# Kernel tuning notes

Hardware: AMD Instinct MI355X
Metric: run time of the kernel (lower is better)

Reference implementation:

```python
import jax, jax.numpy as jnp
import numpy as np

B, C_IN, H, W = 16, 256, 64, 64
D, K = 128, 1024  # embed_dim, nb_entries


def setup_inputs() -> dict:
    key = jax.random.key(0)
    k1, k2, k3, k4 = jax.random.split(key, 4)
    x = jax.random.normal(k1, (B, C_IN, H, W), dtype=jnp.float32)
    conv_w = jax.random.normal(k2, (C_IN, D), dtype=jnp.float32) * 0.05
    conv_b = jax.random.normal(k3, (D,), dtype=jnp.float32) * 0.05
    embed = jax.random.normal(k4, (D, K), dtype=jnp.float32)
    return {"x": x, "conv_w": conv_w, "conv_b": conv_b, "embed": embed}


def reference(x, conv_w, conv_b, embed):
    # 1x1 conv == per-pixel matmul; go straight to NHWC layout.
    z = jnp.einsum('bchw,cd->bhwd', x, conv_w) + conv_b        # [B,H,W,D]
    flat = z.reshape(-1, D)                                     # [N,D]
    # Squared-euclidean distances to codebook columns (||f||^2 - 2 f.E + ||e||^2).
    dist = (jnp.sum(flat * flat, axis=1, keepdims=True)
            - 2.0 * (flat @ embed)
            + jnp.sum(embed * embed, axis=0, keepdims=True))    # [N,K]
    embed_ind = jnp.argmin(dist, axis=1)                        # [N] int
    embed_ind = embed_ind.reshape(B, H, W)
    quantize = jnp.take(embed.T, embed_ind, axis=0)             # [B,H,W,D] gather
    diff = jnp.mean((jax.lax.stop_gradient(quantize) - z) ** 2)
    quantize = z + jax.lax.stop_gradient(quantize - z)          # straight-through
    return quantize.transpose(0, 3, 1, 2), diff, embed_ind
```

## Files before the change

### kernel.cpp

```cpp
#include <hip/hip_runtime.h>

typedef __attribute__((ext_vector_type(4))) float f32x4;
typedef __attribute__((ext_vector_type(8))) short bf16x8;

constexpr int CIN = 256;
constexpr int D   = 128;
constexpr int K   = 1024;
constexpr int HW  = 4096;
constexpr int MT  = 128;
constexpr int DIFF_OFF = 8388608;
constexpr int IDX_OFF  = 8388609;

__device__ float g_scratch[16 + K];
__device__ __align__(16) uint4 g_efrags[64 * 8 * 64];
__device__ __align__(16) uint4 g_wfrags[8 * 8 * 3 * 64];
__device__ __align__(16) float g_embedT[K * D];

__device__ inline unsigned short f2bf(float f) {
    unsigned u = __float_as_uint(f);
    u = u + 0x7fff + ((u >> 16) & 1);
    return (unsigned short)(u >> 16);
}
__device__ inline float bf2f(unsigned short h) {
    return __uint_as_float(((unsigned)h) << 16);
}
__device__ inline void split3(float v, short& a, short& b, short& c) {
    unsigned short h = f2bf(v); float r1 = v - bf2f(h);
    unsigned short m = f2bf(r1); float r2 = r1 - bf2f(m);
    a = (short)h; b = (short)m; c = (short)f2bf(r2);
}
__device__ inline void split3t(float v, short& a, short& b, short& c) {
    unsigned u1 = __float_as_uint(v) & 0xffff0000u;
    float r1 = v - __uint_as_float(u1);
    unsigned u2 = __float_as_uint(r1) & 0xffff0000u;
    float r2 = r1 - __uint_as_float(u2);
    a = (short)(u1 >> 16); b = (short)(u2 >> 16);
    c = (short)(__float_as_uint(r2) >> 16);
}

__device__ inline void gload_lds16(const uint4* g, uint4* l) {
    __builtin_amdgcn_global_load_lds(
        (const __attribute__((address_space(1))) unsigned int*)g,
        (__attribute__((address_space(3))) unsigned int*)l,
        16, 0, 0);
}

__global__ void vq_prep_all(const float* __restrict__ embed,
                            const float* __restrict__ conv_w) {
    const int bi = blockIdx.x;
    const int t  = threadIdx.x;
    if (bi < 128) {
        __shared__ float tile[32][33];
        int kb = bi >> 2, db = bi & 3;
        int tk = t & 31, td = t >> 5;
        #pragma unroll
        for (int dd = 0; dd < 4; ++dd)
            tile[td * 4 + dd][tk] =
                embed[(size_t)(db * 32 + td * 4 + dd) * K + kb * 32 + tk];
        __syncthreads();
        #pragma unroll
        for (int dd = 0; dd < 4; ++dd)
            g_embedT[(size_t)(kb * 32 + td * 4 + dd) * D + db * 32 + tk] =
                tile[tk][td * 4 + dd];
    } else if (bi < 192) {
        int kt = bi - 128, dc = t >> 6, l = t & 63;
        int k  = kt * 16 + (l & 15);
        int d0 = dc * 32 + (l >> 4) * 8;
        unsigned short hi[8], lo[8];
        #pragma unroll
        for (int j = 0; j < 8; ++j) {
            float v = embed[(size_t)(d0 + j) * K + k];
            hi[j] = f2bf(v);
            lo[j] = f2bf(v - bf2f(hi[j]));
        }
        uint4 H, L;
        H.x = (unsigned)hi[0] | ((unsigned)hi[1] << 16);
        H.y = (unsigned)hi[2] | ((unsigned)hi[3] << 16);
        H.z = (unsigned)hi[4] | ((unsigned)hi[5] << 16);
        H.w = (unsigned)hi[6] | ((unsigned)hi[7] << 16);
        L.x = (unsigned)lo[0] | ((unsigned)lo[1] << 16);
        L.y = (unsigned)lo[2] | ((unsigned)lo[3] << 16);
        L.z = (unsigned)lo[4] | ((unsigned)lo[5] << 16);
        L.w = (unsigned)lo[6] | ((unsigned)lo[7] << 16);
        g_efrags[(kt * 8 + dc * 2 + 0) * 64 + l] = H;
        g_efrags[(kt * 8 + dc * 2 + 1) * 64 + l] = L;
    } else if (bi < 208) {
        int old = (bi - 192) * 4 + (t >> 6), l = t & 63;
        int cb = old >> 3, db = old & 7;
        int c0 = cb * 32 + (l >> 4) * 8, d = db * 16 + (l & 15);
        short s1[8], s2[8], s3[8];
        #pragma unroll
        for (int j = 0; j < 8; ++j)
            split3(conv_w[(size_t)(c0 + j) * D + d], s1[j], s2[j], s3[j]);
        #pragma unroll
        for (int s = 0; s < 3; ++s) {
            const short* sp = s == 0 ? s1 : s == 1 ? s2 : s3;
            uint4 P;
            P.x = (unsigned)(unsigned short)sp[0] | ((unsigned)(unsigned short)sp[1] << 16);
            P.y = (unsigned)(unsigned short)sp[2] | ((unsigned)(unsigned short)sp[3] << 16);
            P.z = (unsigned)(unsigned short)sp[4] | ((unsigned)(unsigned short)sp[5] << 16);
            P.w = (unsigned)(unsigned short)sp[6] | ((unsigned)(unsigned short)sp[7] << 16);
            g_wfrags[((cb * 8 + db) * 3 + s) * 64 + l] = P;
        }
    } else {
        int k = (bi - 208) * 256 + t;
        if (k == 0) g_scratch[0] = 0.0f;
        float s = 0.0f;
        for (int d = 0; d < D; ++d) { float v = embed[d * K + k]; s += v * v; }
        g_scratch[16 + k] = s;
    }
}

#define MFMA(a, bb, c) __builtin_amdgcn_mfma_f32_16x16x32_bf16(a, bb, c, 0, 0, 0)

__global__ __launch_bounds__(256, 2) void vq_main(
    const float* __restrict__ x, const float* __restrict__ conv_b,
    float* __restrict__ out)
{
    __shared__ __align__(16) uint4 ebuf[4096];
    __shared__ float e2_s[K];
    __shared__ float tbuf[4 * 16 * 36];
    __shared__ int   ks_s[MT];
    __shared__ float red_s[4];

    const int t    = threadIdx.x;
    const int lane = t & 63;
    const int w    = t >> 6;
    const int wg   = blockIdx.x;
    const int n0   = wg * MT;
    const int b    = n0 >> 12;
    const int hw0  = n0 & 4095;
    const int pxb  = w * 32;
    const int lp   = lane & 15;
    const int lg   = lane >> 4;

    for (int k = t; k < K; k += 256) e2_s[k] = g_scratch[16 + k];

    f32x4 Cz[2][8];
    #pragma unroll
    for (int db = 0; db < 8; ++db) {
        float bv = conv_b[db * 16 + lp];
        Cz[0][db] = (f32x4){bv, bv, bv, bv};
        Cz[1][db] = Cz[0][db];
    }
    {
        #pragma unroll
        for (int i = 0; i < 6; ++i)
            gload_lds16(&g_wfrags[(w * 6 + i) * 64 + lane], &ebuf[(w * 6 + i) * 64]);
        asm volatile("s_waitcnt vmcnt(0)" ::: "memory");
        __syncthreads();

        const float* xl = x + (size_t)b * CIN * HW + (size_t)(lg * 8) * HW
                          + hw0 + pxb + lp;
        for (int cb = 0; cb < 8; ++cb) {
            float v[2][8];
            #pragma unroll
            for (int rb = 0; rb < 2; ++rb)
                #pragma unroll
                for (int j = 0; j < 8; ++j)
                    v[rb][j] = xl[(size_t)(cb * 32 + j) * HW + rb * 16];
            if (cb < 7) {
                const uint4* wsrc = g_wfrags + (size_t)(cb + 1) * 1536;
                uint4* wdst = ebuf + ((cb + 1) & 1) * 1536;
                #pragma unroll
                for (int i = 0; i < 6; ++i)
                    gload_lds16(&wsrc[(w * 6 + i) * 64 + lane], &wdst[(w * 6 + i) * 64]);
            }
            bf16x8 X1[2], X2[2], X3[2];
            #pragma unroll
            for (int rb = 0; rb < 2; ++rb)
                #pragma unroll
                for (int j = 0; j < 8; ++j) {
                    short a, bb, c;
                    split3t(v[rb][j], a, bb, c);
                    X1[rb][j] = a; X2[rb][j] = bb; X3[rb][j] = c;
                }
            const uint4* wb = ebuf + (cb & 1) * 1536;
            #pragma unroll
            for (int db = 0; db < 8; ++db) {
                bf16x8 W1 = *(const bf16x8*)&wb[(db * 3 + 0) * 64 + lane];
                bf16x8 W2 = *(const bf16x8*)&wb[(db * 3 + 1) * 64 + lane];
                bf16x8 W3 = *(const bf16x8*)&wb[(db * 3 + 2) * 64 + lane];
                Cz[0][db] = MFMA(X1[0], W1, Cz[0][db]);
                Cz[1][db] = MFMA(X1[1], W1, Cz[1][db]);
                Cz[0][db] = MFMA(X1[0], W2, Cz[0][db]);
                Cz[1][db] = MFMA(X1[1], W2, Cz[1][db]);
                Cz[0][db] = MFMA(X2[0], W1, Cz[0][db]);
                Cz[1][db] = MFMA(X2[1], W1, Cz[1][db]);
                Cz[0][db] = MFMA(X1[0], W3, Cz[0][db]);
                Cz[1][db] = MFMA(X1[1], W3, Cz[1][db]);
                Cz[0][db] = MFMA(X2[0], W2, Cz[0][db]);
                Cz[1][db] = MFMA(X2[1], W2, Cz[1][db]);
                Cz[0][db] = MFMA(X3[0], W1, Cz[0][db]);
                Cz[1][db] = MFMA(X3[1], W1, Cz[1][db]);
            }
            asm volatile("s_waitcnt vmcnt(0)" ::: "memory");
            __syncthreads();
        }
    }

    bf16x8 A2h[2][4], A2l[2][4];
    {
        float* tb = tbuf + w * 576;
        #pragma unroll
        for (int rb = 0; rb < 2; ++rb) {
            #pragma unroll
            for (int dc = 0; dc < 4; ++dc) {
                #pragma unroll
                for (int h = 0; h < 2; ++h)
                    #pragma unroll
                    for (int r = 0; r < 4; ++r)
                        tb[(lg * 4 + r) * 36 + h * 16 + lp] = Cz[rb][dc * 2 + h][r];
                asm volatile("s_waitcnt lgkmcnt(0)" ::: "memory");
                f32x4 a0 = *(const f32x4*)&tb[lp * 36 + lg * 8];
                f32x4 a1 = *(const f32x4*)&tb[lp * 36 + lg * 8 + 4];
                #pragma unroll
                for (int j = 0; j < 8; ++j) {
                    float zv = -2.0f * (j < 4 ? a0[j] : a1[j - 4]);
                    unsigned short hb = f2bf(zv);
                    A2h[rb][dc][j] = (short)hb;
                    A2l[rb][dc][j] = (short)f2bf(zv - bf2f(hb));
                }
                asm volatile("s_waitcnt lgkmcnt(0)" ::: "memory");
            }
        }
    }

    const uint4* gfr = g_efrags;
    {
        #pragma unroll
        for (int i = 0; i < 8; ++i)
            gload_lds16(&gfr[(w * 8 + i) * 64 + lane], &ebuf[(w * 8 + i) * 64]);
        asm volatile("s_waitcnt vmcnt(0)" ::: "memory");
        __syncthreads();
    }

    float v1[8], v2[8]; int i1[8], i2[8];
    #pragma unroll
    for (int q = 0; q < 8; ++q) { v1[q] = 3.4e38f; v2[q] = 3.4e38f; i1[q] = 0; i2[q] = 0; }

    for (int c = 0; c < 16; ++c) {
        if (c < 15) {
            const uint4* esrc = gfr + (size_t)(c + 1) * 2048;
            uint4* edst = ebuf + ((c + 1) & 1) * 2048;
            #pragma unroll
            for (int i = 0; i < 8; ++i)
                gload_lds16(&esrc[(w * 8 + i) * 64 + lane], &edst[(w * 8 + i) * 64]);
        }
        const bf16x8* eb = (const bf16x8*)&ebuf[(c & 1) * 2048];
        #pragma unroll
        for (int ktl = 0; ktl < 4; ++ktl) {
            int kt = c * 4 + ktl;
            bf16x8 Bh[4], Bl[4];
            #pragma unroll
            for (int dc = 0; dc < 4; ++dc) {
                Bh[dc] = eb[(ktl * 8 + dc * 2 + 0) * 64 + lane];
                Bl[dc] = eb[(ktl * 8 + dc * 2 + 1) * 64 + lane];
            }
            float e2v = e2_s[kt * 16 + lp];
            f32x4 C0 = (f32x4){e2v, e2v, e2v, e2v};
            f32x4 C1 = C0;
            __builtin_amdgcn_s_setprio(1);
            #pragma unroll
            for (int dc = 0; dc < 4; ++dc) {
                C0 = MFMA(A2h[0][dc], Bh[dc], C0);
                C1 = MFMA(A2h[1][dc], Bh[dc], C1);
                C0 = MFMA(A2l[0][dc], Bh[dc], C0);
                C1 = MFMA(A2l[1][dc], Bh[dc], C1);
                C0 = MFMA(A2h[0][dc], Bl[dc], C0);
                C1 = MFMA(A2h[1][dc], Bl[dc], C1);
            }
            __builtin_amdgcn_s_setprio(0);
            int kk = kt * 16 + lp;
            #pragma unroll
            for (int rb = 0; rb < 2; ++rb) {
                f32x4 C = rb ? C1 : C0;
                #pragma unroll
                for (int r = 0; r < 4; ++r) {
                    int q = rb * 4 + r;
                    float s = C[r];
                    bool lt1 = s < v1[q], lt2 = s < v2[q];
                    v2[q] = lt1 ? v1[q] : (lt2 ? s  : v2[q]);
                    i2[q] = lt1 ? i1[q] : (lt2 ? kk : i2[q]);
                    v1[q] = lt1 ? s  : v1[q];
                    i1[q] = lt1 ? kk : i1[q];
                }
            }
        }
        if (c < 15) asm volatile("s_waitcnt vmcnt(0)" ::: "memory");
        __syncthreads();
    }

    #pragma unroll
    for (int off = 1; off < 16; off <<= 1) {
        #pragma unroll
        for (int q = 0; q < 8; ++q) {
            float b1 = __shfl_xor(v1[q], off); int bi1 = __shfl_xor(i1[q], off);
            float b2 = __shfl_xor(v2[q], off); int bi2 = __shfl_xor(i2[q], off);
            bool bf = (b1 < v1[q]) || (b1 == v1[q] && bi1 < i1[q]);
            float cv = bf ? v1[q] : b1;  int ci = bf ? i1[q] : bi1;
            float wv = bf ? b2 : v2[q];  int wi = bf ? bi2 : i2[q];
            v1[q] = bf ? b1 : v1[q];     i1[q] = bf ? bi1 : i1[q];
            bool c2 = (cv < wv) || (cv == wv && ci < wi);
            v2[q] = c2 ? cv : wv;        i2[q] = c2 ? ci : wi;
        }
    }

    float dacc = 0.0f;
    #pragma unroll
    for (int q = 0; q < 8; ++q) {
        const int rb = q >> 2, r = q & 3;
        const int k1 = i1[q], k2 = i2[q];
        float s1 = 0.0f, s2 = 0.0f;
        #pragma unroll
        for (int db = 0; db < 8; ++db) {
            float zv = Cz[rb][db][r];
            s1 += zv * g_embedT[(size_t)k1 * D + db * 16 + lp];
            s2 += zv * g_embedT[(size_t)k2 * D + db * 16 + lp];
        }
        #pragma unroll
        for (int off = 1; off < 16; off <<= 1) {
            s1 += __shfl_xor(s1, off);
            s2 += __shfl_xor(s2, off);
        }
        float d1 = e2_s[k1] - 2.0f * s1;
        float d2 = e2_s[k2] - 2.0f * s2;
        bool p2 = (d2 < d1) || (d2 == d1 && k2 < k1);
        int ks = p2 ? k2 : k1;
        #pragma unroll
        for (int db = 0; db < 8; ++db) {
            float zv = Cz[rb][db][r];
            float qv = g_embedT[(size_t)ks * D + db * 16 + lp];
            float df = qv - zv;
            dacc += df * df;
        }
        if (lp == 0) {
            int px = pxb + rb * 16 + lg * 4 + r;
            ks_s[px] = ks;
            out[IDX_OFF + n0 + px] = (float)ks;
        }
    }
    #pragma unroll
    for (int off = 1; off <= 32; off <<= 1) dacc += __shfl_xor(dacc, off);
    if (lane == 0) red_s[w] = dacc;
    __syncthreads();

    {
        int px = t & 127, half = t >> 7;
        int ks = ks_s[px];
        const f32x4* ep = (const f32x4*)&g_embedT[(size_t)ks * D + half * 64];
        float* ob = out + (size_t)b * D * HW + hw0 + px;
        #pragma unroll
        for (int d4 = 0; d4 < 16; ++d4) {
            f32x4 q4 = ep[d4];
            int d = half * 64 + d4 * 4;
            #pragma unroll
            for (int cc = 0; cc < 4; ++cc)
                ob[(size_t)(d + cc) * HW] = q4[cc];
        }
    }
    if (t == 0) atomicAdd(&g_scratch[0], red_s[0] + red_s[1] + red_s[2] + red_s[3]);
}

__global__ void vq_final(float* __restrict__ out) {
    out[DIFF_OFF] = g_scratch[0] / 8388608.0f;
}

extern "C" void kernel_launch(void* const* d_in, const int* in_sizes, int n_in,
                              void* d_out, int out_size, void* d_ws, size_t ws_size,
                              hipStream_t stream) {
    const float* x      = (const float*)d_in[0];
    const float* conv_w = (const float*)d_in[1];
    const float* conv_b = (const float*)d_in[2];
    const float* embed  = (const float*)d_in[3];
    float* out = (float*)d_out;

    vq_prep_all<<<212, 256, 0, stream>>>(embed, conv_w);
    vq_main    <<<512, 256, 0, stream>>>(x, conv_b, out);
    vq_final   <<<1,   1,   0, stream>>>(out);
}
```

Before: 93.95 us.

## Use single-bf16 distance MFMA with packed-index top-4 and exact top-6 rescoring

Drops the split-bf16 hi/lo correction terms in the distance GEMM, so it issues a third of the MFMAs and loads half the codebook fragment bytes. Candidate tracking changes from two value/index pairs to four floats that carry the codebook index in their low mantissa bits, updated with min/med3 operations. After a cross-lane merge into a top-6 list, the six candidates are rescored in fp32. Accuracy now rests on the true argmin landing among the approximate top candidates, and the +512 offset keeps distances positive so the bit-packed float ordering holds.

```diff
diff --git a/kernel.cpp b/kernel.cpp
--- a/kernel.cpp
+++ b/kernel.cpp
@@ -12,7 +12,7 @@
 constexpr int IDX_OFF  = 8388609;
 
 __device__ float g_scratch[16 + K];
-__device__ __align__(16) uint4 g_efrags[64 * 8 * 64];
+__device__ __align__(16) uint4 g_efrags[64 * 4 * 64];
 __device__ __align__(16) uint4 g_wfrags[8 * 8 * 3 * 64];
 __device__ __align__(16) float g_embedT[K * D];
 
@@ -36,6 +36,15 @@
     float r2 = r1 - __uint_as_float(u2);
     a = (short)(u1 >> 16); b = (short)(u2 >> 16);
     c = (short)(__float_as_uint(r2) >> 16);
+}
+__device__ inline float med3f(float a, float b, float c) {
+    return fmaxf(fminf(a, b), fminf(fmaxf(a, b), c));
+}
+__device__ inline float min3f(float a, float b, float c) {
+    return fminf(fminf(a, b), c);
+}
+__device__ inline float packk(float s, int kk) {
+    return __uint_as_float((__float_as_uint(s) & 0xFFFFFC00u) | (unsigned)kk);
 }
 
 __device__ inline void gload_lds16(const uint4* g, uint4* l) {
@@ -66,24 +75,16 @@
         int kt = bi - 128, dc = t >> 6, l = t & 63;
         int k  = kt * 16 + (l & 15);
         int d0 = dc * 32 + (l >> 4) * 8;
-        unsigned short hi[8], lo[8];
-        #pragma unroll
-        for (int j = 0; j < 8; ++j) {
-            float v = embed[(size_t)(d0 + j) * K + k];
-            hi[j] = f2bf(v);
-            lo[j] = f2bf(v - bf2f(hi[j]));
-        }
-        uint4 H, L;
+        unsigned short hi[8];
+        #pragma unroll
+        for (int j = 0; j < 8; ++j)
+            hi[j] = f2bf(embed[(size_t)(d0 + j) * K + k]);
+        uint4 H;
         H.x = (unsigned)hi[0] | ((unsigned)hi[1] << 16);
         H.y = (unsigned)hi[2] | ((unsigned)hi[3] << 16);
         H.z = (unsigned)hi[4] | ((unsigned)hi[5] << 16);
         H.w = (unsigned)hi[6] | ((unsigned)hi[7] << 16);
-        L.x = (unsigned)lo[0] | ((unsigned)lo[1] << 16);
-        L.y = (unsigned)lo[2] | ((unsigned)lo[3] << 16);
-        L.z = (unsigned)lo[4] | ((unsigned)lo[5] << 16);
-        L.w = (unsigned)lo[6] | ((unsigned)lo[7] << 16);
-        g_efrags[(kt * 8 + dc * 2 + 0) * 64 + l] = H;
-        g_efrags[(kt * 8 + dc * 2 + 1) * 64 + l] = L;
+        g_efrags[(kt * 4 + dc) * 64 + l] = H;
     } else if (bi < 208) {
         int old = (bi - 192) * 4 + (t >> 6), l = t & 63;
         int cb = old >> 3, db = old & 7;
@@ -133,6 +134,7 @@
     const int pxb  = w * 32;
     const int lp   = lane & 15;
     const int lg   = lane >> 4;
+    const float INF = __uint_as_float(0x7f800000u);
 
     for (int k = t; k < K; k += 256) e2_s[k] = g_scratch[16 + k];
 
@@ -199,7 +201,7 @@
         }
     }
 
-    bf16x8 A2h[2][4], A2l[2][4];
+    bf16x8 A2h[2][4];
     {
         float* tb = tbuf + w * 576;
         #pragma unroll
@@ -215,12 +217,8 @@
                 f32x4 a0 = *(const f32x4*)&tb[lp * 36 + lg * 8];
                 f32x4 a1 = *(const f32x4*)&tb[lp * 36 + lg * 8 + 4];
                 #pragma unroll
-                for (int j = 0; j < 8; ++j) {
-                    float zv = -2.0f * (j < 4 ? a0[j] : a1[j - 4]);
-                    unsigned short hb = f2bf(zv);
-                    A2h[rb][dc][j] = (short)hb;
-                    A2l[rb][dc][j] = (short)f2bf(zv - bf2f(hb));
-                }
+                for (int j = 0; j < 8; ++j)
+                    A2h[rb][dc][j] = (short)f2bf(-2.0f * (j < 4 ? a0[j] : a1[j - 4]));
                 asm volatile("s_waitcnt lgkmcnt(0)" ::: "memory");
             }
         }
@@ -235,12 +233,12 @@
         __syncthreads();
     }
 
-    float v1[8], v2[8]; int i1[8], i2[8];
+    float v1[8], v2[8], v3[8], v4[8];
     #pragma unroll
-    for (int q = 0; q < 8; ++q) { v1[q] = 3.4e38f; v2[q] = 3.4e38f; i1[q] = 0; i2[q] = 0; }
-
-    for (int c = 0; c < 16; ++c) {
-        if (c < 15) {
+    for (int q = 0; q < 8; ++q) { v1[q] = INF; v2[q] = INF; v3[q] = INF; v4[q] = INF; }
+
+    for (int c = 0; c < 8; ++c) {
+        if (c < 7) {
             const uint4* esrc = gfr + (size_t)(c + 1) * 2048;
             uint4* edst = ebuf + ((c + 1) & 1) * 2048;
             #pragma unroll
@@ -249,15 +247,13 @@
         }
         const bf16x8* eb = (const bf16x8*)&ebuf[(c & 1) * 2048];
         #pragma unroll
-        for (int ktl = 0; ktl < 4; ++ktl) {
-            int kt = c * 4 + ktl;
-            bf16x8 Bh[4], Bl[4];
-            #pragma unroll
-            for (int dc = 0; dc < 4; ++dc) {
-                Bh[dc] = eb[(ktl * 8 + dc * 2 + 0) * 64 + lane];
-                Bl[dc] = eb[(ktl * 8 + dc * 2 + 1) * 64 + lane];
-            }
-            float e2v = e2_s[kt * 16 + lp];
+        for (int ktl = 0; ktl < 8; ++ktl) {
+            int kt = c * 8 + ktl;
+            bf16x8 Bh[4];
+            #pragma unroll
+            for (int dc = 0; dc < 4; ++dc)
+                Bh[dc] = eb[(ktl * 4 + dc) * 64 + lane];
+            float e2v = e2_s[kt * 16 + lp] + 512.0f;
             f32x4 C0 = (f32x4){e2v, e2v, e2v, e2v};
             f32x4 C1 = C0;
             __builtin_amdgcn_s_setprio(1);
@@ -265,10 +261,6 @@
             for (int dc = 0; dc < 4; ++dc) {
                 C0 = MFMA(A2h[0][dc], Bh[dc], C0);
                 C1 = MFMA(A2h[1][dc], Bh[dc], C1);
-                C0 = MFMA(A2l[0][dc], Bh[dc], C0);
-                C1 = MFMA(A2l[1][dc], Bh[dc], C1);
-                C0 = MFMA(A2h[0][dc], Bl[dc], C0);
-                C1 = MFMA(A2h[1][dc], Bl[dc], C1);
             }
             __builtin_amdgcn_s_setprio(0);
             int kk = kt * 16 + lp;
@@ -278,66 +270,71 @@
                 #pragma unroll
                 for (int r = 0; r < 4; ++r) {
                     int q = rb * 4 + r;
-                    float s = C[r];
-                    bool lt1 = s < v1[q], lt2 = s < v2[q];
-                    v2[q] = lt1 ? v1[q] : (lt2 ? s  : v2[q]);
-                    i2[q] = lt1 ? i1[q] : (lt2 ? kk : i2[q]);
-                    v1[q] = lt1 ? s  : v1[q];
-                    i1[q] = lt1 ? kk : i1[q];
+                    float s = packk(C[r], kk);
+                    float t1 = fminf(v1[q], s);
+                    float t2 = med3f(s, v1[q], v2[q]);
+                    float t3 = med3f(s, v2[q], v3[q]);
+                    float t4 = med3f(s, v3[q], v4[q]);
+                    v1[q] = t1; v2[q] = t2; v3[q] = t3; v4[q] = t4;
                 }
             }
         }
-        if (c < 15) asm volatile("s_waitcnt vmcnt(0)" ::: "memory");
+        if (c < 7) asm volatile("s_waitcnt vmcnt(0)" ::: "memory");
         __syncthreads();
-    }
-
-    #pragma unroll
-    for (int off = 1; off < 16; off <<= 1) {
-        #pragma unroll
-        for (int q = 0; q < 8; ++q) {
-            float b1 = __shfl_xor(v1[q], off); int bi1 = __shfl_xor(i1[q], off);
-            float b2 = __shfl_xor(v2[q], off); int bi2 = __shfl_xor(i2[q], off);
-            bool bf = (b1 < v1[q]) || (b1 == v1[q] && bi1 < i1[q]);
-            float cv = bf ? v1[q] : b1;  int ci = bf ? i1[q] : bi1;
-            float wv = bf ? b2 : v2[q];  int wi = bf ? bi2 : i2[q];
-            v1[q] = bf ? b1 : v1[q];     i1[q] = bf ? bi1 : i1[q];
-            bool c2 = (cv < wv) || (cv == wv && ci < wi);
-            v2[q] = c2 ? cv : wv;        i2[q] = c2 ? ci : wi;
-        }
     }
 
     float dacc = 0.0f;
     #pragma unroll
     for (int q = 0; q < 8; ++q) {
         const int rb = q >> 2, r = q & 3;
-        const int k1 = i1[q], k2 = i2[q];
-        float s1 = 0.0f, s2 = 0.0f;
+        float a1 = v1[q], a2 = v2[q], a3 = v3[q], a4 = v4[q], a5 = INF, a6 = INF;
+        #pragma unroll
+        for (int off = 1; off < 16; off <<= 1) {
+            float b1 = __shfl_xor(a1, off), b2 = __shfl_xor(a2, off);
+            float b3 = __shfl_xor(a3, off), b4 = __shfl_xor(a4, off);
+            float b5 = __shfl_xor(a5, off), b6 = __shfl_xor(a6, off);
+            float m11 = fmaxf(a1, b1);
+            float m12 = fmaxf(a1, b2), m21 = fmaxf(a2, b1);
+            float m13 = fmaxf(a1, b3), m22 = fmaxf(a2, b2), m31 = fmaxf(a3, b1);
+            float m14 = fmaxf(a1, b4), m23 = fmaxf(a2, b3), m32 = fmaxf(a3, b2), m41 = fmaxf(a4, b1);
+            float m15 = fmaxf(a1, b5), m24 = fmaxf(a2, b4), m33 = fmaxf(a3, b3), m42 = fmaxf(a4, b2), m51 = fmaxf(a5, b1);
+            float c1 = fminf(a1, b1);
+            float c2 = min3f(a2, b2, m11);
+            float c3 = fminf(min3f(a3, b3, m12), m21);
+            float c4 = fminf(min3f(a4, b4, m13), fminf(m22, m31));
+            float c5 = fminf(min3f(a5, b5, m14), min3f(m23, m32, m41));
+            float c6 = fminf(fminf(min3f(a6, b6, m15), min3f(m24, m33, m42)), m51);
+            a1 = c1; a2 = c2; a3 = c3; a4 = c4; a5 = c5; a6 = c6;
+        }
+        float cm[6] = {a1, a2, a3, a4, a5, a6};
+        float bd = 0.0f; int bk = 0;
+        #pragma unroll
+        for (int j = 0; j < 6; ++j) {
+            int kc = (int)(__float_as_uint(cm[j]) & 1023u);
+            float sum = 0.0f;
+            #pragma unroll
+            for (int db = 0; db < 8; ++db)
+                sum += Cz[rb][db][r] * g_embedT[(size_t)kc * D + db * 16 + lp];
+            #pragma unroll
+            for (int off = 1; off < 16; off <<= 1) sum += __shfl_xor(sum, off);
+            float de = e2_s[kc] - 2.0f * sum;
+            if (j == 0) { bd = de; bk = kc; }
+            else {
+                bool upd = (de < bd) || (de == bd && kc < bk);
+                bd = upd ? de : bd;
+                bk = upd ? kc : bk;
+            }
+        }
         #pragma unroll
         for (int db = 0; db < 8; ++db) {
-            float zv = Cz[rb][db][r];
-            s1 += zv * g_embedT[(size_t)k1 * D + db * 16 + lp];
-            s2 += zv * g_embedT[(size_t)k2 * D + db * 16 + lp];
-        }
-        #pragma unroll
-        for (int off = 1; off < 16; off <<= 1) {
-            s1 += __shfl_xor(s1, off);
-            s2 += __shfl_xor(s2, off);
-        }
-        float d1 = e2_s[k1] - 2.0f * s1;
-        float d2 = e2_s[k2] - 2.0f * s2;
-        bool p2 = (d2 < d1) || (d2 == d1 && k2 < k1);
-        int ks = p2 ? k2 : k1;
-        #pragma unroll
-        for (int db = 0; db < 8; ++db) {
-            float zv = Cz[rb][db][r];
-            float qv = g_embedT[(size_t)ks * D + db * 16 + lp];
-            float df = qv - zv;
+            float qv = g_embedT[(size_t)bk * D + db * 16 + lp];
+            float df = qv - Cz[rb][db][r];
             dacc += df * df;
         }
         if (lp == 0) {
             int px = pxb + rb * 16 + lg * 4 + r;
-            ks_s[px] = ks;
-            out[IDX_OFF + n0 + px] = (float)ks;
+            ks_s[px] = bk;
+            out[IDX_OFF + n0 + px] = (float)bk;
         }
     }
     #pragma unroll
```

Result: slower. 98.53 us (+4.9%).
